# Performance work log

Measured on AMD Instinct MI355X. Metric: run time of the kernel, lower is better.

The kernel has to match this reference:

```python
import jax, jax.numpy as jnp
import numpy as np

D_MODEL = 1024
N_HEADS = 16
D_K = D_MODEL // N_HEADS
B, T = 2, 2048


def setup_inputs() -> dict:
    key = jax.random.key(0)
    ks = jax.random.split(key, 12)
    s = 0.02
    return {
        "q": jax.random.normal(ks[0], (B, T, D_MODEL), jnp.float32),
        "k": jax.random.normal(ks[1], (B, T, D_MODEL), jnp.float32),
        "v": jax.random.normal(ks[2], (B, T, D_MODEL), jnp.float32),
        "Wq": jax.random.normal(ks[3], (D_MODEL, D_MODEL), jnp.float32) * s,
        "bq": jnp.zeros((D_MODEL,), jnp.float32),
        "Wk": jax.random.normal(ks[4], (D_MODEL, D_MODEL), jnp.float32) * s,
        "bk": jnp.zeros((D_MODEL,), jnp.float32),
        "Wv": jax.random.normal(ks[5], (D_MODEL, D_MODEL), jnp.float32) * s,
        "bv": jnp.zeros((D_MODEL,), jnp.float32),
        "Wo": jax.random.normal(ks[6], (D_MODEL, D_MODEL), jnp.float32) * s,
        "bo": jnp.zeros((D_MODEL,), jnp.float32),
        "mask": jnp.ones((B, T), jnp.int32),
        "causal": 1,
    }


def reference(q, k, v, Wq, bq, Wk, bk, Wv, bv, Wo, bo, mask, causal):
    Bq, Tq, D = q.shape
    Tk = k.shape[1]
    # projections (torch Linear: x @ W.T + b), split heads -> [B, H, T, d_k]
    qh = (q @ Wq.T + bq).reshape(Bq, Tq, N_HEADS, D_K).transpose(0, 2, 1, 3)
    kh = (k @ Wk.T + bk).reshape(Bq, Tk, N_HEADS, D_K).transpose(0, 2, 1, 3)
    vh = (v @ Wv.T + bv).reshape(Bq, Tk, N_HEADS, D_K).transpose(0, 2, 1, 3)
    scores = jnp.einsum("bhqd,bhkd->bhqk", qh, kh) / jnp.sqrt(jnp.float32(D_K))
    neg_inf = jnp.float32(-jnp.inf)
    if mask is not None:
        scores = jnp.where(mask[:, None, None, :] == 0, neg_inf, scores)
    if causal:
        causal_mask = jnp.tril(jnp.ones((Tq, Tq), jnp.float32))
        scores = jnp.where(causal_mask == 0, neg_inf, scores)
    attn = jax.nn.softmax(scores, axis=-1)
    out = jnp.einsum("bhqk,bhkd->bhqd", attn, vh)
    out = out.transpose(0, 2, 1, 3).reshape(Bq, Tq, D)
    return out @ Wo.T + bo
```

## Files before the change

kernel.cpp:

```cpp
#include <hip/hip_runtime.h>
#include <cstdint>
#include <cstddef>


typedef __bf16 bf16x8 __attribute__((ext_vector_type(8)));
typedef __bf16 bf16x4 __attribute__((ext_vector_type(4)));
typedef float f32x4 __attribute__((ext_vector_type(4)));

#define MFMA(a, b, c) __builtin_amdgcn_mfma_f32_16x16x32_bf16((a), (b), (c), 0, 0, 0)

static constexpr int D_MODEL = 1024;
static constexpr int T_ = 2048;
static constexpr int M_TOK = 4096;

__device__ __forceinline__ unsigned short f32_to_bf16(float f) {
    union { float f; uint32_t u; } v; v.f = f;
    uint32_t u = v.u;
    uint32_t r = u + 0x7fffu + ((u >> 16) & 1u);
    return (unsigned short)(r >> 16);
}
__device__ __forceinline__ unsigned f32_to_bf16_fast(float f) {
    union { float f; uint32_t u; } v; v.f = f;
    return (v.u + 0x8000u) >> 16;
}

typedef __attribute__((address_space(1))) void* as1_ptr;
typedef __attribute__((address_space(3))) void* as3_ptr;
__device__ __forceinline__ void gload_lds16(const void* g, void* l) {
    __builtin_amdgcn_global_load_lds((as1_ptr)(void*)g, (as3_ptr)l, 16, 0, 0);
}

__global__ __launch_bounds__(256) void cvt_all(
    const float* __restrict__ q, const float* __restrict__ k,
    const float* __restrict__ v, const float* __restrict__ wq,
    const float* __restrict__ wk, const float* __restrict__ wv,
    const float* __restrict__ wo, ushort4* __restrict__ dst) {
    int i = blockIdx.x * blockDim.x + threadIdx.x;
    constexpr int R = 1 << 20;
    const float* s;
    int idx;
    if (i < 3 * R) {
        s = (i < R) ? q : (i < 2 * R) ? k : v;
        idx = i & (R - 1);
    } else {
        int j = i - 3 * R;
        int w = j >> 18;
        s = (w == 0) ? wq : (w == 1) ? wk : (w == 2) ? wv : wo;
        idx = j & ((1 << 18) - 1);
    }
    float4 f = ((const float4*)s)[idx];
    ushort4 o;
    o.x = (unsigned short)f32_to_bf16(f.x); o.y = (unsigned short)f32_to_bf16(f.y);
    o.z = (unsigned short)f32_to_bf16(f.z); o.w = (unsigned short)f32_to_bf16(f.w);
    dst[i] = o;
}

template<int MODE>
__device__ __forceinline__ void gemm_body(
    const unsigned short* __restrict__ A, const unsigned short* __restrict__ W,
    const float* __restrict__ bias, void* __restrict__ outp,
    unsigned short* As, unsigned short* Ws, int bx, int by)
{
    const int tid = threadIdx.x;
    const int lane = tid & 63, wave = tid >> 6;
    const int wm = wave >> 1, wn = wave & 1;
    const int r16 = lane & 15, kg = lane >> 4;
    const int m_blk = by * 128, n_blk = bx * 64;

    f32x4 acc[4][2];
    #pragma unroll
    for (int mt = 0; mt < 4; ++mt)
        #pragma unroll
        for (int nt = 0; nt < 2; ++nt) acc[mt][nt] = (f32x4){0, 0, 0, 0};

    for (int k0 = 0; k0 < D_MODEL; k0 += 64) {
        __syncthreads();
        #pragma unroll
        for (int j = 0; j < 4; ++j) {
            int si = j * 256 + tid;
            int row = si >> 3, cg = (si & 7) ^ (row & 7);
            gload_lds16(A + (size_t)(m_blk + row) * D_MODEL + k0 + cg * 8,
                        (char*)As + (j * 256 + wave * 64) * 16);
        }
        #pragma unroll
        for (int j = 0; j < 2; ++j) {
            int si = j * 256 + tid;
            int row = si >> 3, cg = (si & 7) ^ (row & 7);
            gload_lds16(W + (size_t)(n_blk + row) * D_MODEL + k0 + cg * 8,
                        (char*)Ws + (j * 256 + wave * 64) * 16);
        }
        __syncthreads();
        #pragma unroll
        for (int kc = 0; kc < 2; ++kc) {
            bf16x8 af[4], wf[2];
            #pragma unroll
            for (int mt = 0; mt < 4; ++mt) {
                int row = wm * 64 + mt * 16 + r16;
                af[mt] = *(const bf16x8*)(As + row * 64 + (((kc * 4 + kg) ^ (row & 7)) * 8));
            }
            #pragma unroll
            for (int nt = 0; nt < 2; ++nt) {
                int row = wn * 32 + nt * 16 + r16;
                wf[nt] = *(const bf16x8*)(Ws + row * 64 + (((kc * 4 + kg) ^ (row & 7)) * 8));
            }
            #pragma unroll
            for (int mt = 0; mt < 4; ++mt)
                #pragma unroll
                for (int nt = 0; nt < 2; ++nt)
                    acc[mt][nt] = MFMA(af[mt], wf[nt], acc[mt][nt]);
        }
    }
    #pragma unroll
    for (int nt = 0; nt < 2; ++nt) {
        int n = n_blk + wn * 32 + nt * 16 + r16;
        float bn = bias[n];
        #pragma unroll
        for (int mt = 0; mt < 4; ++mt)
            #pragma unroll
            for (int r = 0; r < 4; ++r) {
                int m = m_blk + wm * 64 + mt * 16 + kg * 4 + r;
                float vv = acc[mt][nt][r] + bn;
                if (MODE == 3) {
                    ((float*)outp)[(size_t)m * D_MODEL + n] = vv;
                } else {
                    int b = m >> 11, t = m & 2047, h = n >> 6, dki = n & 63;
                    unsigned short* o = (unsigned short*)outp;
                    if (MODE == 0)
                        o[((size_t)(b * 16 + h) * 2048 + t) * 64 + dki] = f32_to_bf16(vv);
                    else
                        o[((size_t)(b * 16 + h) * 64 + dki) * 2048 + t] = f32_to_bf16(vv);
                }
            }
    }
}

__global__ __launch_bounds__(256) void gemm_qkv(
    const unsigned short* __restrict__ qb, const unsigned short* __restrict__ kb,
    const unsigned short* __restrict__ vb, const unsigned short* __restrict__ Wqb,
    const unsigned short* __restrict__ Wkb, const unsigned short* __restrict__ Wvb,
    const float* __restrict__ bq, const float* __restrict__ bk, const float* __restrict__ bv,
    unsigned short* __restrict__ Qhp, unsigned short* __restrict__ Khp,
    unsigned short* __restrict__ Vtp)
{
    __shared__ __align__(16) unsigned short As[128 * 64];
    __shared__ __align__(16) unsigned short Ws[64 * 64];
    const int z = blockIdx.z;
    const unsigned short* A = (z == 0) ? qb : (z == 1) ? kb : vb;
    const unsigned short* W = (z == 0) ? Wqb : (z == 1) ? Wkb : Wvb;
    const float* bias = (z == 0) ? bq : (z == 1) ? bk : bv;
    if (z < 2)
        gemm_body<0>(A, W, bias, (z == 0) ? (void*)Qhp : (void*)Khp, As, Ws,
                     blockIdx.x, blockIdx.y);
    else
        gemm_body<2>(A, W, bias, (void*)Vtp, As, Ws, blockIdx.x, blockIdx.y);
}

__global__ __launch_bounds__(256) void gemm_out(
    const unsigned short* __restrict__ ab, const unsigned short* __restrict__ Wob,
    const float* __restrict__ bo, float* __restrict__ outp)
{
    __shared__ __align__(16) unsigned short As[128 * 64];
    __shared__ __align__(16) unsigned short Ws[64 * 64];
    gemm_body<3>(ab, Wob, bo, (void*)outp, As, Ws, blockIdx.x, blockIdx.y);
}

__global__ __launch_bounds__(256) void attn_fwd(
    const unsigned short* __restrict__ Qh, const unsigned short* __restrict__ Kh,
    const unsigned short* __restrict__ Vt, const int* __restrict__ mask,
    const int* __restrict__ causal_p, unsigned short* __restrict__ attnout)
{
    __shared__ __align__(16) unsigned short Ks[2][64 * 64];
    __shared__ __align__(16) unsigned short Vs[2][64 * 64];

    const int tid = threadIdx.x;
    const int lane = tid & 63, wave = tid >> 6;
    const int p = blockIdx.x, bh = blockIdx.y;
    const int b = bh >> 4, h = bh & 15;
    const int causal = *causal_p;
    const int r16 = lane & 15, kg = lane >> 4;

    const int qcA = p, qcB = 31 - p;
    const int q0A = qcA * 64 + wave * 16;
    const int q0B = qcB * 64 + wave * 16;

    const unsigned short* Qb = Qh + (size_t)bh * T_ * 64;
    const unsigned short* Kb = Kh + (size_t)bh * T_ * 64;
    const unsigned short* Vb = Vt + (size_t)bh * 64 * T_;
    const int* mb = mask + b * T_;

    bf16x8 qfA0 = *(const bf16x8*)(Qb + (size_t)(q0A + r16) * 64 + kg * 8);
    bf16x8 qfA1 = *(const bf16x8*)(Qb + (size_t)(q0A + r16) * 64 + 32 + kg * 8);
    bf16x8 qfB0 = *(const bf16x8*)(Qb + (size_t)(q0B + r16) * 64 + kg * 8);
    bf16x8 qfB1 = *(const bf16x8*)(Qb + (size_t)(q0B + r16) * 64 + 32 + kg * 8);

    float lA = 0.f, lB = 0.f;
    f32x4 oA[4], oB[4];
    #pragma unroll
    for (int f = 0; f < 4; ++f) { oA[f] = (f32x4){0,0,0,0}; oB[f] = (f32x4){0,0,0,0}; }
    const float sc2 = 0.18033688011112042f;
    const int lim = wave * 16 + r16;

    const int nT = causal ? (qcB + 1) : 32;

    auto stage = [&](int buf, int t) {
        int t0 = t * 64;
        #pragma unroll
        for (int j = 0; j < 2; ++j) {
            int si = j * 256 + tid;
            int row = si >> 3, cg = (si & 7) ^ (row & 7);
            gload_lds16(Kb + (size_t)(t0 + row) * 64 + cg * 8,
                        (char*)Ks[buf] + (j * 256 + wave * 64) * 16);
            gload_lds16(Vb + (size_t)row * T_ + t0 + cg * 8,
                        (char*)Vs[buf] + (j * 256 + wave * 64) * 16);
        }
    };

    stage(0, 0);
    for (int t = 0; t < nT; ++t) {
        __syncthreads();
        if (t + 1 < nT) stage((t + 1) & 1, t + 1);
        const unsigned short* Kst = Ks[t & 1];
        const unsigned short* Vst = Vs[t & 1];
        const int t0 = t * 64;
        const bool activeA = !causal || (t <= qcA);
        const bool needcA = causal && (t == qcA);
        const bool needcB = causal && (t == qcB);

        unsigned long long km = __ballot(mb[t0 + lane] != 0);

        f32x4 sA[4], sB[4];
        #pragma unroll
        for (int c = 0; c < 4; ++c) {
            int key = c * 16 + r16;
            bf16x8 kf0 = *(const bf16x8*)(Kst + key * 64 + ((kg ^ (key & 7)) * 8));
            bf16x8 kf1 = *(const bf16x8*)(Kst + key * 64 + (((4 + kg) ^ (key & 7)) * 8));
            f32x4 zB = (f32x4){0,0,0,0};
            zB = MFMA(kf0, qfB0, zB);
            zB = MFMA(kf1, qfB1, zB);
            sB[c] = zB;
            if (activeA) {
                f32x4 zA = (f32x4){0,0,0,0};
                zA = MFMA(kf0, qfA0, zA);
                zA = MFMA(kf1, qfA1, zA);
                sA[c] = zA;
            }
        }

        union pk_t { unsigned u[4]; bf16x8 v; };
        pk_t paA[2], paB[2];
        #pragma unroll
        for (int c = 0; c < 4; ++c) {
            unsigned mc = (unsigned)(km >> (c * 16));
            float pBv[4], pAv[4];
            #pragma unroll
            for (int r = 0; r < 4; ++r) {
                int kbit = kg * 4 + r;
                bool mk = (mc >> kbit) & 1;
                int kk = c * 16 + kbit;
                bool okB = mk && (!needcB || (kk <= lim));
                float eB = okB ? __builtin_amdgcn_exp2f(sB[c][r] * sc2) : 0.f;
                pBv[r] = eB; lB += eB;
                if (activeA) {
                    bool okA = mk && (!needcA || (kk <= lim));
                    float eA = okA ? __builtin_amdgcn_exp2f(sA[c][r] * sc2) : 0.f;
                    pAv[r] = eA; lA += eA;
                }
            }
            int half = (c & 1) * 2;
            paB[c >> 1].u[half]     = f32_to_bf16_fast(pBv[0]) | (f32_to_bf16_fast(pBv[1]) << 16);
            paB[c >> 1].u[half + 1] = f32_to_bf16_fast(pBv[2]) | (f32_to_bf16_fast(pBv[3]) << 16);
            if (activeA) {
                paA[c >> 1].u[half]     = f32_to_bf16_fast(pAv[0]) | (f32_to_bf16_fast(pAv[1]) << 16);
                paA[c >> 1].u[half + 1] = f32_to_bf16_fast(pAv[2]) | (f32_to_bf16_fast(pAv[3]) << 16);
            }
        }

        #pragma unroll
        for (int f = 0; f < 4; ++f) {
            int row = f * 16 + r16;
            int rx = row & 7;
            #pragma unroll
            for (int cp = 0; cp < 2; ++cp) {
                int g0 = (cp * 2) * 2 + (kg >> 1);
                int g1 = (cp * 2 + 1) * 2 + (kg >> 1);
                union { bf16x4 h[2]; bf16x8 v; } vf;
                vf.h[0] = *(const bf16x4*)(Vst + row * 64 + ((g0 ^ rx) * 8) + (kg & 1) * 4);
                vf.h[1] = *(const bf16x4*)(Vst + row * 64 + ((g1 ^ rx) * 8) + (kg & 1) * 4);
                oB[f] = MFMA(paB[cp].v, vf.v, oB[f]);
                if (activeA) oA[f] = MFMA(paA[cp].v, vf.v, oA[f]);
            }
        }
    }

    lA += __shfl_xor(lA, 16, 64); lA += __shfl_xor(lA, 32, 64);
    lB += __shfl_xor(lB, 16, 64); lB += __shfl_xor(lB, 32, 64);
    float invA = (lA > 0.f) ? 1.0f / lA : 0.f;
    float invB = (lB > 0.f) ? 1.0f / lB : 0.f;
    #pragma unroll
    for (int r = 0; r < 4; ++r) {
        int ql = kg * 4 + r;
        float iA = __shfl(invA, ql, 64);
        float iB = __shfl(invB, ql, 64);
        size_t baseA = ((size_t)(b * T_ + q0A + ql)) * D_MODEL + h * 64;
        size_t baseB = ((size_t)(b * T_ + q0B + ql)) * D_MODEL + h * 64;
        #pragma unroll
        for (int f = 0; f < 4; ++f) {
            attnout[baseA + f * 16 + r16] = f32_to_bf16(oA[f][r] * iA);
            attnout[baseB + f * 16 + r16] = f32_to_bf16(oB[f][r] * iB);
        }
    }
}

extern "C" void kernel_launch(void* const* d_in, const int* in_sizes, int n_in,
                              void* d_out, int out_size, void* d_ws, size_t ws_size,
                              hipStream_t stream) {
    const float* q  = (const float*)d_in[0];
    const float* k  = (const float*)d_in[1];
    const float* v  = (const float*)d_in[2];
    const float* Wq = (const float*)d_in[3];
    const float* bq = (const float*)d_in[4];
    const float* Wk = (const float*)d_in[5];
    const float* bk = (const float*)d_in[6];
    const float* Wv = (const float*)d_in[7];
    const float* bv = (const float*)d_in[8];
    const float* Wo = (const float*)d_in[9];
    const float* bo = (const float*)d_in[10];
    const int* mask   = (const int*)d_in[11];
    const int* causal = (const int*)d_in[12];

    const size_t SZ_TOK = (size_t)M_TOK * D_MODEL;
    const size_t SZ_W   = (size_t)D_MODEL * D_MODEL;

    unsigned short* qb  = (unsigned short*)d_ws;
    unsigned short* kb  = qb  + SZ_TOK;
    unsigned short* vb  = kb  + SZ_TOK;
    unsigned short* Wqb = vb  + SZ_TOK;
    unsigned short* Wkb = Wqb + SZ_W;
    unsigned short* Wvb = Wkb + SZ_W;
    unsigned short* Wob = Wvb + SZ_W;
    unsigned short* Qhp = Wob + SZ_W;
    unsigned short* Khp = Qhp + SZ_TOK;
    unsigned short* Vtp = Khp + SZ_TOK;
    unsigned short* ab  = Vtp + SZ_TOK;

    cvt_all<<<16384, 256, 0, stream>>>(q, k, v, Wq, Wk, Wv, Wo, (ushort4*)qb);

    gemm_qkv<<<dim3(D_MODEL / 64, M_TOK / 128, 3), 256, 0, stream>>>(
        qb, kb, vb, Wqb, Wkb, Wvb, bq, bk, bv, Qhp, Khp, Vtp);

    attn_fwd<<<dim3(16, 32), 256, 0, stream>>>(Qhp, Khp, Vtp, mask, causal, ab);

    gemm_out<<<dim3(D_MODEL / 64, M_TOK / 128), 256, 0, stream>>>(ab, Wob, bo,
                                                                  (float*)d_out);
}
```

Baseline: 249.4 us.

## Vectorize GEMM epilogues via swapped MFMA operands and split attention into per-tile blocks

Q and K projections now swap the MFMA operands so that each lane holds four consecutive output columns. This lets them write packed ushort4 rows in token-major [B,T,D] layout, and the output GEMM writes float4, replacing scattered scalar stores. The attention kernel reads Q and K with a stride of D_MODEL directly from that layout. It also drops the paired A/B query-tile scheme in favour of one query tile per block, with a 32x32 grid ordered so heavy and light causal tiles interleave. The cost is losing the shared K/V staging between two query tiles, and more blocks with uneven work.

```diff
diff --git a/kernel.cpp b/kernel.cpp
--- a/kernel.cpp
+++ b/kernel.cpp
@@ -61,6 +61,7 @@
     const float* __restrict__ bias, void* __restrict__ outp,
     unsigned short* As, unsigned short* Ws, int bx, int by)
 {
+    constexpr bool SWAP = (MODE != 2);
     const int tid = threadIdx.x;
     const int lane = tid & 63, wave = tid >> 6;
     const int wm = wave >> 1, wn = wave & 1;
@@ -107,30 +108,52 @@
             for (int mt = 0; mt < 4; ++mt)
                 #pragma unroll
                 for (int nt = 0; nt < 2; ++nt)
-                    acc[mt][nt] = MFMA(af[mt], wf[nt], acc[mt][nt]);
-        }
-    }
-    #pragma unroll
-    for (int nt = 0; nt < 2; ++nt) {
-        int n = n_blk + wn * 32 + nt * 16 + r16;
-        float bn = bias[n];
-        #pragma unroll
-        for (int mt = 0; mt < 4; ++mt)
-            #pragma unroll
-            for (int r = 0; r < 4; ++r) {
-                int m = m_blk + wm * 64 + mt * 16 + kg * 4 + r;
-                float vv = acc[mt][nt][r] + bn;
+                    acc[mt][nt] = SWAP ? MFMA(wf[nt], af[mt], acc[mt][nt])
+                                       : MFMA(af[mt], wf[nt], acc[mt][nt]);
+        }
+    }
+    if (MODE == 2) {
+        #pragma unroll
+        for (int nt = 0; nt < 2; ++nt) {
+            int n = n_blk + wn * 32 + nt * 16 + r16;
+            float bn = bias[n];
+            int hh = n >> 6, dki = n & 63;
+            #pragma unroll
+            for (int mt = 0; mt < 4; ++mt) {
+                int m0 = m_blk + wm * 64 + mt * 16 + kg * 4;
+                int bb = m0 >> 11, ti = m0 & 2047;
+                ushort4 pk;
+                pk.x = f32_to_bf16(acc[mt][nt][0] + bn);
+                pk.y = f32_to_bf16(acc[mt][nt][1] + bn);
+                pk.z = f32_to_bf16(acc[mt][nt][2] + bn);
+                pk.w = f32_to_bf16(acc[mt][nt][3] + bn);
+                *(ushort4*)((unsigned short*)outp +
+                    ((size_t)(bb * 16 + hh) * 64 + dki) * 2048 + ti) = pk;
+            }
+        }
+    } else {
+        #pragma unroll
+        for (int nt = 0; nt < 2; ++nt) {
+            int n0 = n_blk + wn * 32 + nt * 16 + kg * 4;
+            float4 bn4 = *(const float4*)(bias + n0);
+            #pragma unroll
+            for (int mt = 0; mt < 4; ++mt) {
+                int m = m_blk + wm * 64 + mt * 16 + r16;
                 if (MODE == 3) {
-                    ((float*)outp)[(size_t)m * D_MODEL + n] = vv;
+                    float4 st;
+                    st.x = acc[mt][nt][0] + bn4.x; st.y = acc[mt][nt][1] + bn4.y;
+                    st.z = acc[mt][nt][2] + bn4.z; st.w = acc[mt][nt][3] + bn4.w;
+                    *(float4*)((float*)outp + (size_t)m * D_MODEL + n0) = st;
                 } else {
-                    int b = m >> 11, t = m & 2047, h = n >> 6, dki = n & 63;
-                    unsigned short* o = (unsigned short*)outp;
-                    if (MODE == 0)
-                        o[((size_t)(b * 16 + h) * 2048 + t) * 64 + dki] = f32_to_bf16(vv);
-                    else
-                        o[((size_t)(b * 16 + h) * 64 + dki) * 2048 + t] = f32_to_bf16(vv);
+                    ushort4 pk;
+                    pk.x = f32_to_bf16(acc[mt][nt][0] + bn4.x);
+                    pk.y = f32_to_bf16(acc[mt][nt][1] + bn4.y);
+                    pk.z = f32_to_bf16(acc[mt][nt][2] + bn4.z);
+                    pk.w = f32_to_bf16(acc[mt][nt][3] + bn4.w);
+                    *(ushort4*)((unsigned short*)outp + (size_t)m * D_MODEL + n0) = pk;
                 }
             }
+        }
     }
 }
 
@@ -174,33 +197,32 @@
 
     const int tid = threadIdx.x;
     const int lane = tid & 63, wave = tid >> 6;
-    const int p = blockIdx.x, bh = blockIdx.y;
+    const int bh = blockIdx.x;
+    const int y = blockIdx.y, y0 = y & 7, j4 = y >> 3;
+    const int qc = (j4 == 0) ? y0 : (j4 == 1) ? (15 - y0)
+                 : (j4 == 2) ? (16 + y0) : (31 - y0);
     const int b = bh >> 4, h = bh & 15;
     const int causal = *causal_p;
     const int r16 = lane & 15, kg = lane >> 4;
 
-    const int qcA = p, qcB = 31 - p;
-    const int q0A = qcA * 64 + wave * 16;
-    const int q0B = qcB * 64 + wave * 16;
-
-    const unsigned short* Qb = Qh + (size_t)bh * T_ * 64;
-    const unsigned short* Kb = Kh + (size_t)bh * T_ * 64;
+    const int q0 = qc * 64 + wave * 16;
+
+    const unsigned short* Qb = Qh + (size_t)b * T_ * D_MODEL + h * 64;
+    const unsigned short* Kb = Kh + (size_t)b * T_ * D_MODEL + h * 64;
     const unsigned short* Vb = Vt + (size_t)bh * 64 * T_;
     const int* mb = mask + b * T_;
 
-    bf16x8 qfA0 = *(const bf16x8*)(Qb + (size_t)(q0A + r16) * 64 + kg * 8);
-    bf16x8 qfA1 = *(const bf16x8*)(Qb + (size_t)(q0A + r16) * 64 + 32 + kg * 8);
-    bf16x8 qfB0 = *(const bf16x8*)(Qb + (size_t)(q0B + r16) * 64 + kg * 8);
-    bf16x8 qfB1 = *(const bf16x8*)(Qb + (size_t)(q0B + r16) * 64 + 32 + kg * 8);
-
-    float lA = 0.f, lB = 0.f;
-    f32x4 oA[4], oB[4];
+    bf16x8 qf0 = *(const bf16x8*)(Qb + (size_t)(q0 + r16) * D_MODEL + kg * 8);
+    bf16x8 qf1 = *(const bf16x8*)(Qb + (size_t)(q0 + r16) * D_MODEL + 32 + kg * 8);
+
+    float l = 0.f;
+    f32x4 o[4];
     #pragma unroll
-    for (int f = 0; f < 4; ++f) { oA[f] = (f32x4){0,0,0,0}; oB[f] = (f32x4){0,0,0,0}; }
+    for (int f = 0; f < 4; ++f) o[f] = (f32x4){0, 0, 0, 0};
     const float sc2 = 0.18033688011112042f;
     const int lim = wave * 16 + r16;
 
-    const int nT = causal ? (qcB + 1) : 32;
+    const int nT = causal ? (qc + 1) : 32;
 
     auto stage = [&](int buf, int t) {
         int t0 = t * 64;
@@ -208,7 +230,7 @@
         for (int j = 0; j < 2; ++j) {
             int si = j * 256 + tid;
             int row = si >> 3, cg = (si & 7) ^ (row & 7);
-            gload_lds16(Kb + (size_t)(t0 + row) * 64 + cg * 8,
+            gload_lds16(Kb + (size_t)(t0 + row) * D_MODEL + cg * 8,
                         (char*)Ks[buf] + (j * 256 + wave * 64) * 16);
             gload_lds16(Vb + (size_t)row * T_ + t0 + cg * 8,
                         (char*)Vs[buf] + (j * 256 + wave * 64) * 16);
@@ -222,57 +244,40 @@
         const unsigned short* Kst = Ks[t & 1];
         const unsigned short* Vst = Vs[t & 1];
         const int t0 = t * 64;
-        const bool activeA = !causal || (t <= qcA);
-        const bool needcA = causal && (t == qcA);
-        const bool needcB = causal && (t == qcB);
+        const bool needc = causal && (t == qc);
 
         unsigned long long km = __ballot(mb[t0 + lane] != 0);
 
-        f32x4 sA[4], sB[4];
+        f32x4 s[4];
         #pragma unroll
         for (int c = 0; c < 4; ++c) {
             int key = c * 16 + r16;
             bf16x8 kf0 = *(const bf16x8*)(Kst + key * 64 + ((kg ^ (key & 7)) * 8));
             bf16x8 kf1 = *(const bf16x8*)(Kst + key * 64 + (((4 + kg) ^ (key & 7)) * 8));
-            f32x4 zB = (f32x4){0,0,0,0};
-            zB = MFMA(kf0, qfB0, zB);
-            zB = MFMA(kf1, qfB1, zB);
-            sB[c] = zB;
-            if (activeA) {
-                f32x4 zA = (f32x4){0,0,0,0};
-                zA = MFMA(kf0, qfA0, zA);
-                zA = MFMA(kf1, qfA1, zA);
-                sA[c] = zA;
-            }
+            f32x4 z = (f32x4){0, 0, 0, 0};
+            z = MFMA(kf0, qf0, z);
+            z = MFMA(kf1, qf1, z);
+            s[c] = z;
         }
 
         union pk_t { unsigned u[4]; bf16x8 v; };
-        pk_t paA[2], paB[2];
+        pk_t pa[2];
         #pragma unroll
         for (int c = 0; c < 4; ++c) {
             unsigned mc = (unsigned)(km >> (c * 16));
-            float pBv[4], pAv[4];
+            float pv[4];
             #pragma unroll
             for (int r = 0; r < 4; ++r) {
                 int kbit = kg * 4 + r;
                 bool mk = (mc >> kbit) & 1;
                 int kk = c * 16 + kbit;
-                bool okB = mk && (!needcB || (kk <= lim));
-                float eB = okB ? __builtin_amdgcn_exp2f(sB[c][r] * sc2) : 0.f;
-                pBv[r] = eB; lB += eB;
-                if (activeA) {
-                    bool okA = mk && (!needcA || (kk <= lim));
-                    float eA = okA ? __builtin_amdgcn_exp2f(sA[c][r] * sc2) : 0.f;
-                    pAv[r] = eA; lA += eA;
-                }
+                bool ok = mk && (!needc || (kk <= lim));
+                float e = ok ? __builtin_amdgcn_exp2f(s[c][r] * sc2) : 0.f;
+                pv[r] = e; l += e;
             }
             int half = (c & 1) * 2;
-            paB[c >> 1].u[half]     = f32_to_bf16_fast(pBv[0]) | (f32_to_bf16_fast(pBv[1]) << 16);
-            paB[c >> 1].u[half + 1] = f32_to_bf16_fast(pBv[2]) | (f32_to_bf16_fast(pBv[3]) << 16);
-            if (activeA) {
-                paA[c >> 1].u[half]     = f32_to_bf16_fast(pAv[0]) | (f32_to_bf16_fast(pAv[1]) << 16);
-                paA[c >> 1].u[half + 1] = f32_to_bf16_fast(pAv[2]) | (f32_to_bf16_fast(pAv[3]) << 16);
-            }
+            pa[c >> 1].u[half]     = f32_to_bf16_fast(pv[0]) | (f32_to_bf16_fast(pv[1]) << 16);
+            pa[c >> 1].u[half + 1] = f32_to_bf16_fast(pv[2]) | (f32_to_bf16_fast(pv[3]) << 16);
         }
 
         #pragma unroll
@@ -286,28 +291,21 @@
                 union { bf16x4 h[2]; bf16x8 v; } vf;
                 vf.h[0] = *(const bf16x4*)(Vst + row * 64 + ((g0 ^ rx) * 8) + (kg & 1) * 4);
                 vf.h[1] = *(const bf16x4*)(Vst + row * 64 + ((g1 ^ rx) * 8) + (kg & 1) * 4);
-                oB[f] = MFMA(paB[cp].v, vf.v, oB[f]);
-                if (activeA) oA[f] = MFMA(paA[cp].v, vf.v, oA[f]);
-            }
-        }
-    }
-
-    lA += __shfl_xor(lA, 16, 64); lA += __shfl_xor(lA, 32, 64);
-    lB += __shfl_xor(lB, 16, 64); lB += __shfl_xor(lB, 32, 64);
-    float invA = (lA > 0.f) ? 1.0f / lA : 0.f;
-    float invB = (lB > 0.f) ? 1.0f / lB : 0.f;
+                o[f] = MFMA(pa[cp].v, vf.v, o[f]);
+            }
+        }
+    }
+
+    l += __shfl_xor(l, 16, 64); l += __shfl_xor(l, 32, 64);
+    float inv = (l > 0.f) ? 1.0f / l : 0.f;
     #pragma unroll
     for (int r = 0; r < 4; ++r) {
         int ql = kg * 4 + r;
-        float iA = __shfl(invA, ql, 64);
-        float iB = __shfl(invB, ql, 64);
-        size_t baseA = ((size_t)(b * T_ + q0A + ql)) * D_MODEL + h * 64;
-        size_t baseB = ((size_t)(b * T_ + q0B + ql)) * D_MODEL + h * 64;
-        #pragma unroll
-        for (int f = 0; f < 4; ++f) {
-            attnout[baseA + f * 16 + r16] = f32_to_bf16(oA[f][r] * iA);
-            attnout[baseB + f * 16 + r16] = f32_to_bf16(oB[f][r] * iB);
-        }
+        float iv = __shfl(inv, ql, 64);
+        size_t base = ((size_t)(b * T_ + q0 + ql)) * D_MODEL + h * 64;
+        #pragma unroll
+        for (int f = 0; f < 4; ++f)
+            attnout[base + f * 16 + r16] = f32_to_bf16(o[f][r] * iv);
     }
 }
 
@@ -348,7 +346,7 @@
     gemm_qkv<<<dim3(D_MODEL / 64, M_TOK / 128, 3), 256, 0, stream>>>(
         qb, kb, vb, Wqb, Wkb, Wvb, bq, bk, bv, Qhp, Khp, Vtp);
 
-    attn_fwd<<<dim3(16, 32), 256, 0, stream>>>(Qhp, Khp, Vtp, mask, causal, ab);
+    attn_fwd<<<dim3(32, 32), 256, 0, stream>>>(Qhp, Khp, Vtp, mask, causal, ab);
 
     gemm_out<<<dim3(D_MODEL / 64, M_TOK / 128), 256, 0, stream>>>(ab, Wob, bo,
                                                                   (float*)d_out);
```

Result: faster. 233.0 us (-6.6%).
